# Optimization experiments

Measured on AMD Instinct MI355X. Metric: run time of the kernel, lower is better.

The kernel has to match this reference:

```python
import jax, jax.numpy as jnp
import numpy as np

EPS = 1e-5

def _bn(x, g, b):
    # training-mode BatchNorm3d over (N, T, H, W) per channel (axis=1), biased variance
    red = (0, 2, 3, 4)
    m = x.mean(red, keepdims=True)
    v = x.var(red, keepdims=True)
    s = (1, -1, 1, 1, 1)
    return (x - m) / jnp.sqrt(v + EPS) * g.reshape(s) + b.reshape(s)

def _conv3d(x, w, b):
    # Conv3d kernel (1,3,3), padding (0,1,1)
    y = jax.lax.conv_general_dilated(x, w, (1, 1, 1), ((0, 0), (1, 1), (1, 1)),
                                     dimension_numbers=('NCDHW', 'OIDHW', 'NCDHW'))
    return y + b[None, :, None, None, None]

def _forward(x1, x2, attn_weight, W_up, b_up, W_mlp, b_mlp, g_mlp, be_mlp,
             W_c1, b_c1, g_c1, be_c1, W_c2, b_c2, g_c2, be_c2):
    w2 = W_up[:, :, 0]  # [Cin, Cout, 2, 2]
    y = jnp.einsum('bcthw,cokl->bothkwl', x1, w2)
    b_, o, t, h, k, w_, l = y.shape
    x1u = y.reshape(b_, o, t, h * k, w_ * l) + b_up[None, :, None, None, None]

    bs, d_in, T, H, W = x2.shape
    nH = attn_weight.shape[0]
    hh, ww = attn_weight.shape[2], attn_weight.shape[3]
    # [nH, bs, h, w, T, T] -> [nH*bs, T*T, h, w], bilinear upsample to (H, W)
    A = attn_weight.transpose(0, 1, 4, 5, 2, 3).reshape(nH * bs, T * T, hh, ww)
    A = jax.image.resize(A, (nH * bs, T * T, H, W), method='linear')
    A = A.reshape(nH, bs, T, T, H, W)
    # per-(head,b,H,W) temporal attention matmul: avoids materializing x2.repeat(n_head,...)
    ctx = jnp.einsum('nbtsxy,bcsxy->btxycn', A, x2)  # [bs,T,H,W,d_in,nH]
    ctx = ctx.reshape(bs, T, H, W, d_in * nH)        # flatten order (c, n) matches torch permute+view
    hmlp = jnp.einsum('btxyk,ko->btxyo', ctx, W_mlp) + b_mlp
    hmlp = hmlp.transpose(0, 4, 1, 2, 3)  # [bs, enc, T, H, W]
    hmlp = jax.nn.relu(_bn(hmlp, g_mlp, be_mlp))

    x = jnp.concatenate([hmlp, x1u], axis=1)  # [bs, enc+dec, T, H, W]
    x = jax.nn.relu(_bn(_conv3d(x, W_c1, b_c1), g_c1, be_c1))
    x = jax.nn.relu(_bn(_conv3d(x, W_c2, b_c2), g_c2, be_c2))
    return x

def setup_inputs() -> dict:
    key = jax.random.key(0)
    ks = jax.random.split(key, 8)
    bs, T, H, W = 2, 8, 128, 128
    dec, enc, nH = 64, 32, 4
    hh = ww = 16  # attn_scale_factor = 8
    return {
        'x1': jax.random.normal(ks[0], (bs, dec, T, H // 2, W // 2), jnp.float32),
        'x2': jax.random.normal(ks[1], (bs, enc, T, H, W), jnp.float32),
        'attn_weight': jax.random.uniform(ks[2], (nH, bs, hh, ww, T, T), jnp.float32),
        'W_up': jax.random.normal(ks[3], (dec, dec, 1, 2, 2), jnp.float32) * 0.05,
        'b_up': jnp.zeros((dec,), jnp.float32),
        'W_mlp': jax.random.normal(ks[4], (nH * enc, enc), jnp.float32) * 0.05,
        'b_mlp': jnp.zeros((enc,), jnp.float32),
        'g_mlp': jnp.ones((enc,), jnp.float32),
        'be_mlp': jnp.zeros((enc,), jnp.float32),
        'W_c1': jax.random.normal(ks[5], (enc, dec + enc, 1, 3, 3), jnp.float32) * 0.05,
        'b_c1': jnp.zeros((enc,), jnp.float32),
        'g_c1': jnp.ones((enc,), jnp.float32),
        'be_c1': jnp.zeros((enc,), jnp.float32),
        'W_c2': jax.random.normal(ks[6], (enc, enc, 1, 3, 3), jnp.float32) * 0.05,
        'b_c2': jnp.zeros((enc,), jnp.float32),
        'g_c2': jnp.ones((enc,), jnp.float32),
        'be_c2': jnp.zeros((enc,), jnp.float32),
    }

def reference(x1, x2, attn_weight, W_up, b_up, W_mlp, b_mlp, g_mlp, be_mlp,
              W_c1, b_c1, g_c1, be_c1, W_c2, b_c2, g_c2, be_c2):
    return _forward(x1, x2, attn_weight, W_up, b_up, W_mlp, b_mlp, g_mlp, be_mlp,
                    W_c1, b_c1, g_c1, be_c1, W_c2, b_c2, g_c2, be_c2)
```

## Files before the change

### kernel.cpp

```cpp
#include <hip/hip_runtime.h>


#define EPSV 1e-5f

typedef __attribute__((ext_vector_type(8))) short short8;
typedef __attribute__((ext_vector_type(4))) short short4v;
typedef __attribute__((ext_vector_type(4))) float floatx4;

__device__ inline short f2bf(float f) {
  union { float f; unsigned u; } v; v.f = f;
  unsigned r = (v.u + 0x7fffu + ((v.u >> 16) & 1u)) >> 16;
  return (short)r;
}
__device__ inline float bf2f(short s) {
  union { unsigned u; float f; } v; v.u = ((unsigned)(unsigned short)s) << 16;
  return v.f;
}

#define UB_OFF   0
#define HMB_OFF  8388608
#define C1B_OFF  12582912
#define C2B_OFF  16777216
#define WB1_OFF  20971520
#define WB2_OFF  20985344
#define WUP_OFF  20989952
#define ST_OFF   20998144
#define SC_OFF   20998336

__global__ __launch_bounds__(256) void k_repackb(const float* __restrict__ Wc1, const float* __restrict__ Wc2,
        const float* __restrict__ Wup,
        short* __restrict__ wb1, short* __restrict__ wb2, short* __restrict__ wupb) {
  int i = blockIdx.x*256 + threadIdx.x;
  if (i < 27648) {
    int cc = i / 9216, r = i % 9216;
    int tap = r / 1024, r2 = r % 1024;
    int nt = r2 >> 9, lane = (r2 >> 3) & 63, j = r2 & 7;
    int o = nt*16 + (lane & 15);
    int cin = cc*32 + (lane >> 4)*8 + j;
    wb1[i] = f2bf(Wc1[(o*96 + cin)*9 + tap]);
  }
  if (i < 9216) {
    int tap = i / 1024, r2 = i % 1024;
    int nt = r2 >> 9, lane = (r2 >> 3) & 63, j = r2 & 7;
    int o = nt*16 + (lane & 15);
    int cin = (lane >> 4)*8 + j;
    wb2[i] = f2bf(Wc2[(o*32 + cin)*9 + tap]);
  }
  if (i < 16384) {
    int j = i & 7, lane = (i >> 3) & 63, r = i >> 9;
    int nt = r & 3, kb = (r >> 2) & 1, p = r >> 3;
    int c = kb*32 + (lane >> 4)*8 + j;
    int o = nt*16 + (lane & 15);
    wupb[i] = f2bf(Wup[(c*64 + o)*4 + p]);
  }
}

__global__ __launch_bounds__(256) void k_up_mfma(const float* __restrict__ x1,
        const short* __restrict__ wupb, const float* __restrict__ bup,
        short* __restrict__ Ub) {
  __shared__ __align__(16) char smem[34816];
  short8* stage = (short8*)smem;
  int t = blockIdx.y, b = blockIdx.z;
  int chunk = blockIdx.x >> 2, parity = blockIdx.x & 3;
  int tid = threadIdx.x, lane = tid & 63, w = tid >> 6;

  {
    const float* xp = x1 + ((long)(b*64)*8 + t)*4096 + chunk*256 + tid;
    #pragma unroll
    for (int o8 = 0; o8 < 8; ++o8) {
      short8 v;
      #pragma unroll
      for (int j = 0; j < 8; ++j) v[j] = f2bf(xp[(long)(o8*8+j)*32768]);
      int kb = o8 >> 2, cq = o8 & 3;
      stage[(kb*16 + (tid>>4))*64 + cq*16 + (tid&15)] = v;
    }
  }
  __syncthreads();

  floatx4 acc[4][4];
  #pragma unroll
  for (int nt=0; nt<4; ++nt) {
    float bb = bup[nt*16 + (lane&15)];
    #pragma unroll
    for (int mt=0; mt<4; ++mt) acc[mt][nt] = (floatx4){bb,bb,bb,bb};
  }
  const short8* wp = (const short8*)wupb;
  #pragma unroll
  for (int kb=0; kb<2; ++kb) {
    short8 bfr[4];
    #pragma unroll
    for (int nt=0; nt<4; ++nt) bfr[nt] = wp[((parity*2+kb)*4+nt)*64 + lane];
    #pragma unroll
    for (int mt=0; mt<4; ++mt) {
      short8 a = stage[(kb*16 + w*4 + mt)*64 + lane];
      #pragma unroll
      for (int nt=0; nt<4; ++nt)
        acc[mt][nt] = __builtin_amdgcn_mfma_f32_16x16x32_bf16(a, bfr[nt], acc[mt][nt], 0,0,0);
    }
  }

  __syncthreads();
  short* trb = (short*)smem;
  #pragma unroll
  for (int mt=0; mt<4; ++mt)
    #pragma unroll
    for (int nt=0; nt<4; ++nt)
      #pragma unroll
      for (int r=0; r<4; ++r)
        trb[(w*64 + mt*16 + (lane>>4)*4 + r)*68 + nt*16 + (lane&15)] = f2bf(acc[mt][nt][r]);
  __syncthreads();

  int ip = chunk*256 + tid;
  int X = 2*(ip>>6) + (parity>>1), Y = 2*(ip&63) + (parity&1);
  short* dst = Ub + (((long)(b*8+t)*16384 + X*128 + Y)*64);
  const short* src = trb + tid*68;
  #pragma unroll
  for (int k=0; k<16; ++k)
    *(short4v*)(dst + k*4) = *(const short4v*)(src + k*4);
}

__global__ __launch_bounds__(256) void k_ctxmlp(const float* __restrict__ x2,
        const float* __restrict__ attn, const float* __restrict__ Wmlp,
        const float* __restrict__ bmlp, short* __restrict__ HMb) {
  int t = blockIdx.y, b = blockIdx.z;
  int pos = blockIdx.x*256 + threadIdx.x;
  __shared__ float la[8192];
  float4* la4 = (float4*)la;
  const float4* g4 = (const float4*)attn;
  #pragma unroll
  for (int k=0;k<8;++k) {
    int i = k*256 + (int)threadIdx.x;
    int s4 = i & 1, iy = (i>>1)&15, ix = (i>>5)&15, n = i>>9;
    la4[i] = g4[((((n*2+b)*16+ix)*16+iy)*8+t)*2 + s4];
  }
  __syncthreads();
  int x = pos >> 7, y = pos & 127;
  float ux = (x+0.5f)*0.125f - 0.5f;
  float uy = (y+0.5f)*0.125f - 0.5f;
  int ix0 = (int)floorf(ux), iy0 = (int)floorf(uy);
  float fx = ux - (float)ix0, fy = uy - (float)iy0;
  int ixa = max(ix0,0), ixb = min(ix0+1,15);
  int iya = max(iy0,0), iyb = min(iy0+1,15);
  float w00=(1.f-fx)*(1.f-fy), w01=(1.f-fx)*fy, w10=fx*(1.f-fy), w11=fx*fy;
  float a[4][8];
  #pragma unroll
  for (int n=0;n<4;++n) {
    const float4* p00 = la4 + ((n*16+ixa)*16+iya)*2;
    const float4* p01 = la4 + ((n*16+ixa)*16+iyb)*2;
    const float4* p10 = la4 + ((n*16+ixb)*16+iya)*2;
    const float4* p11 = la4 + ((n*16+ixb)*16+iyb)*2;
    #pragma unroll
    for (int q=0;q<2;++q) {
      float4 c00=p00[q], c01=p01[q], c10=p10[q], c11=p11[q];
      a[n][q*4+0] = w00*c00.x + w01*c01.x + w10*c10.x + w11*c11.x;
      a[n][q*4+1] = w00*c00.y + w01*c01.y + w10*c10.y + w11*c11.y;
      a[n][q*4+2] = w00*c00.z + w01*c01.z + w10*c10.z + w11*c11.z;
      a[n][q*4+3] = w00*c00.w + w01*c01.w + w10*c10.w + w11*c11.w;
    }
  }
  float acc[32];
  #pragma unroll
  for (int o=0;o<32;++o) acc[o] = bmlp[o];
  const float* x2p = x2 + b*4194304 + pos;
  #pragma unroll 4
  for (int c=0;c<32;++c) {
    float xr[8];
    #pragma unroll
    for (int s=0;s<8;++s) xr[s] = x2p[(c*8+s)*16384];
    #pragma unroll
    for (int n=0;n<4;++n) {
      float ctx = 0.f;
      #pragma unroll
      for (int s=0;s<8;++s) ctx = fmaf(a[n][s], xr[s], ctx);
      const float* wrow = Wmlp + (c*4+n)*32;
      #pragma unroll
      for (int o=0;o<32;++o) acc[o] = fmaf(ctx, wrow[o], acc[o]);
    }
  }
  short8* hp = (short8*)(HMb + ((long)((b*8+t)*16384 + pos)) * 32);
  #pragma unroll
  for (int g=0; g<4; ++g) {
    short8 v;
    #pragma unroll
    for (int j=0;j<8;++j) v[j] = f2bf(acc[g*8+j]);
    hp[g] = v;
  }
}

__global__ __launch_bounds__(256) void k_stats_cl(const unsigned* __restrict__ src, float* __restrict__ st) {
  __shared__ float sb[64];
  if (threadIdx.x < 64) sb[threadIdx.x] = 0.f;
  __syncthreads();
  int cp = threadIdx.x & 15;
  int pg = threadIdx.x >> 4;
  long pbase = (long)blockIdx.x * 256;
  float s0=0.f,q0=0.f,s1=0.f,q1=0.f;
  #pragma unroll 4
  for (int it = 0; it < 16; ++it) {
    long pos = pbase + it*16 + pg;
    unsigned d = src[pos*16 + cp];
    float v0 = bf2f((short)(d & 0xffffu));
    float v1 = bf2f((short)(d >> 16));
    s0+=v0; q0+=v0*v0; s1+=v1; q1+=v1*v1;
  }
  s0 += __shfl_xor(s0,16); s0 += __shfl_xor(s0,32);
  q0 += __shfl_xor(q0,16); q0 += __shfl_xor(q0,32);
  s1 += __shfl_xor(s1,16); s1 += __shfl_xor(s1,32);
  q1 += __shfl_xor(q1,16); q1 += __shfl_xor(q1,32);
  if ((threadIdx.x & 63) < 16) {
    atomicAdd(&sb[2*cp],    s0); atomicAdd(&sb[2*cp+1],    s1);
    atomicAdd(&sb[32+2*cp], q0); atomicAdd(&sb[32+2*cp+1], q1);
  }
  __syncthreads();
  if (threadIdx.x < 64) atomicAdd(&st[threadIdx.x], sb[threadIdx.x]);
}

__global__ void k_finalize(const float* __restrict__ st, const float* __restrict__ g,
                           const float* __restrict__ be, float* __restrict__ sc, float* __restrict__ sh) {
  int c = threadIdx.x;
  if (c < 32) {
    float mean = st[c] * (1.f/262144.f);
    float var  = st[32+c] * (1.f/262144.f) - mean*mean;
    float s = g[c] / sqrtf(var + EPSV);
    sc[c] = s;
    sh[c] = be[c] - mean*s;
  }
}

template<int NCHUNK>
__global__ __launch_bounds__(256) void k_conv_mfma(
    const short* __restrict__ srcCL, const short* __restrict__ srcU,
    const short* __restrict__ wb, const float* __restrict__ bias,
    const float* __restrict__ sc, const float* __restrict__ sh,
    short* __restrict__ dstCL, float* __restrict__ st) {
  __shared__ __align__(16) char smem[25920];
  __shared__ float sbuf[64];
  short* stage = (short*)smem;

  int t = blockIdx.y, b = blockIdx.z;
  int x0 = (int)(blockIdx.x >> 3) * 16, y0 = (int)(blockIdx.x & 7) * 16;
  int tid = threadIdx.x, lane = tid & 63, w = tid >> 6;
  if (tid < 64) sbuf[tid] = 0.f;

  float bias0 = bias[lane & 15], bias1 = bias[16 + (lane & 15)];
  floatx4 acc[4][2];
  #pragma unroll
  for (int mt=0; mt<4; ++mt) {
    acc[mt][0] = (floatx4){bias0,bias0,bias0,bias0};
    acc[mt][1] = (floatx4){bias1,bias1,bias1,bias1};
  }
  long slab = (long)(b*8+t)*16384;

  for (int cc=0; cc<NCHUNK; ++cc) {
    __syncthreads();
    if (cc == 0) {
      #pragma unroll
      for (int g=0; g<4; ++g) {
        float s0=sc[g*8+0],s1=sc[g*8+1],s2=sc[g*8+2],s3=sc[g*8+3];
        float s4=sc[g*8+4],s5=sc[g*8+5],s6=sc[g*8+6],s7=sc[g*8+7];
        float h0=sh[g*8+0],h1=sh[g*8+1],h2=sh[g*8+2],h3=sh[g*8+3];
        float h4=sh[g*8+4],h5=sh[g*8+5],h6=sh[g*8+6],h7=sh[g*8+7];
        for (int p=tid; p<324; p+=256) {
          int r = p/18, c = p - r*18;
          int X = x0 - 1 + r, Y = y0 - 1 + c;
          short8 val = (short8)0;
          if ((unsigned)X < 128u && (unsigned)Y < 128u) {
            short8 raw = *(const short8*)(srcCL + ((slab + X*128 + Y) * 32 + g*8));
            val[0]=f2bf(fmaxf(fmaf(bf2f(raw[0]),s0,h0),0.f));
            val[1]=f2bf(fmaxf(fmaf(bf2f(raw[1]),s1,h1),0.f));
            val[2]=f2bf(fmaxf(fmaf(bf2f(raw[2]),s2,h2),0.f));
            val[3]=f2bf(fmaxf(fmaf(bf2f(raw[3]),s3,h3),0.f));
            val[4]=f2bf(fmaxf(fmaf(bf2f(raw[4]),s4,h4),0.f));
            val[5]=f2bf(fmaxf(fmaf(bf2f(raw[5]),s5,h5),0.f));
            val[6]=f2bf(fmaxf(fmaf(bf2f(raw[6]),s6,h6),0.f));
            val[7]=f2bf(fmaxf(fmaf(bf2f(raw[7]),s7,h7),0.f));
          }
          *(short8*)(stage + p*40 + g*8) = val;
        }
      }
    } else {
      int cbase = (cc-1)*32;
      #pragma unroll
      for (int g=0; g<4; ++g) {
        for (int p=tid; p<324; p+=256) {
          int r = p/18, c = p - r*18;
          int X = x0 - 1 + r, Y = y0 - 1 + c;
          short8 val = (short8)0;
          if ((unsigned)X < 128u && (unsigned)Y < 128u) {
            val = *(const short8*)(srcU + ((slab + X*128 + Y) * 64 + cbase + g*8));
          }
          *(short8*)(stage + p*40 + g*8) = val;
        }
      }
    }
    __syncthreads();
    const short8* wbp = (const short8*)wb + (long)cc*9*2*64;
    #pragma unroll
    for (int tap=0; tap<9; ++tap) {
      int dy = tap/3, dx = tap - dy*3;
      short8 b0 = wbp[(tap*2+0)*64 + lane];
      short8 b1 = wbp[(tap*2+1)*64 + lane];
      #pragma unroll
      for (int mt=0; mt<4; ++mt) {
        int p = (w*4 + mt + dy)*18 + (lane & 15) + dx;
        short8 a = *(const short8*)(stage + p*40 + (lane>>4)*8);
        acc[mt][0] = __builtin_amdgcn_mfma_f32_16x16x32_bf16(a, b0, acc[mt][0], 0,0,0);
        acc[mt][1] = __builtin_amdgcn_mfma_f32_16x16x32_bf16(a, b1, acc[mt][1], 0,0,0);
      }
    }
  }

  float s0=0.f,q0=0.f,s1=0.f,q1=0.f;
  #pragma unroll
  for (int mt=0; mt<4; ++mt)
    #pragma unroll
    for (int r=0; r<4; ++r) {
      float v0 = acc[mt][0][r]; s0 += v0; q0 += v0*v0;
      float v1 = acc[mt][1][r]; s1 += v1; q1 += v1*v1;
    }
  s0 += __shfl_xor(s0,16); s0 += __shfl_xor(s0,32);
  q0 += __shfl_xor(q0,16); q0 += __shfl_xor(q0,32);
  s1 += __shfl_xor(s1,16); s1 += __shfl_xor(s1,32);
  q1 += __shfl_xor(q1,16); q1 += __shfl_xor(q1,32);

  __syncthreads();
  if (lane < 16) {
    atomicAdd(&sbuf[lane],    s0); atomicAdd(&sbuf[16+lane], s1);
    atomicAdd(&sbuf[32+lane], q0); atomicAdd(&sbuf[48+lane], q1);
  }
  short* tr = (short*)smem;
  #pragma unroll
  for (int mt=0; mt<4; ++mt) {
    int prow = w*4 + mt;
    #pragma unroll
    for (int nt=0; nt<2; ++nt) {
      #pragma unroll
      for (int r=0; r<4; ++r) {
        int m = (lane>>4)*4 + r;
        tr[(prow*16 + m)*32 + nt*16 + (lane&15)] = f2bf(acc[mt][nt][r]);
      }
    }
  }
  __syncthreads();
  int px = tid >> 4, py = tid & 15;
  short8* d8 = (short8*)(dstCL + ((slab + (long)(x0+px)*128 + (y0+py))*32));
  const short8* s8 = (const short8*)(tr + tid*32);
  d8[0]=s8[0]; d8[1]=s8[1]; d8[2]=s8[2]; d8[3]=s8[3];
  if (tid < 64) atomicAdd(&st[tid], sbuf[tid]);
}

__global__ __launch_bounds__(256) void k_bnrelu2(const short* __restrict__ C2b,
        const float* __restrict__ sc, const float* __restrict__ sh,
        float* __restrict__ out) {
  __shared__ float tb[10592];
  int t = blockIdx.y, b = blockIdx.z;
  int posbase = blockIdx.x * 256;
  int tid = threadIdx.x;
  long slab = (long)(b*8+t)*16384;
  {
    const short8* sp = (const short8*)(C2b + (slab + posbase + tid)*32);
    int pi = tid + (tid>>5)*8;
    #pragma unroll
    for (int g=0; g<4; ++g) {
      short8 v = sp[g];
      #pragma unroll
      for (int j=0; j<8; ++j) {
        int ch = g*8+j;
        tb[ch*321 + pi] = fmaxf(fmaf(bf2f(v[j]), sc[ch], sh[ch]), 0.f);
      }
    }
  }
  __syncthreads();
  int ch = tid >> 3, pg = tid & 7;
  float* op = out + ((long)(b*32+ch)*8 + t)*16384 + posbase + pg*32;
  const float* tp = tb + ch*321 + pg*40;
  #pragma unroll
  for (int k=0; k<8; ++k) {
    float4 v;
    v.x = tp[k*4+0]; v.y = tp[k*4+1]; v.z = tp[k*4+2]; v.w = tp[k*4+3];
    *(float4*)(op + k*4) = v;
  }
}

extern "C" void kernel_launch(void* const* d_in, const int* in_sizes, int n_in,
                              void* d_out, int out_size, void* d_ws, size_t ws_size,
                              hipStream_t stream) {
  (void)in_sizes; (void)n_in; (void)out_size; (void)ws_size;
  const float* x1   = (const float*)d_in[0];
  const float* x2   = (const float*)d_in[1];
  const float* attn = (const float*)d_in[2];
  const float* Wup  = (const float*)d_in[3];
  const float* bup  = (const float*)d_in[4];
  const float* Wmlp = (const float*)d_in[5];
  const float* bmlp = (const float*)d_in[6];
  const float* gmlp = (const float*)d_in[7];
  const float* bemlp= (const float*)d_in[8];
  const float* Wc1  = (const float*)d_in[9];
  const float* bc1  = (const float*)d_in[10];
  const float* gc1  = (const float*)d_in[11];
  const float* bec1 = (const float*)d_in[12];
  const float* Wc2  = (const float*)d_in[13];
  const float* bc2  = (const float*)d_in[14];
  const float* gc2  = (const float*)d_in[15];
  const float* bec2 = (const float*)d_in[16];
  float* ws  = (float*)d_ws;
  float* out = (float*)d_out;

  short* Ub   = (short*)(ws + UB_OFF);
  short* HMb  = (short*)(ws + HMB_OFF);
  short* C1b  = (short*)(ws + C1B_OFF);
  short* C2b  = (short*)(ws + C2B_OFF);
  short* wb1  = (short*)(ws + WB1_OFF);
  short* wb2  = (short*)(ws + WB2_OFF);
  short* wupb = (short*)(ws + WUP_OFF);
  float* st1  = ws + ST_OFF;
  float* st2  = st1 + 64;
  float* st3  = st2 + 64;
  float* sc1  = ws + SC_OFF;  float* sh1 = sc1+32;
  float* sc2  = sh1+32;       float* sh2 = sc2+32;
  float* sc3  = sh2+32;       float* sh3 = sc3+32;

  hipMemsetAsync(st1, 0, 192*sizeof(float), stream);
  k_repackb<<<108, 256, 0, stream>>>(Wc1, Wc2, Wup, wb1, wb2, wupb);
  k_up_mfma<<<dim3(64,8,2), 256, 0, stream>>>(x1, wupb, bup, Ub);
  k_ctxmlp<<<dim3(64,8,2), 256, 0, stream>>>(x2, attn, Wmlp, bmlp, HMb);
  k_stats_cl<<<1024, 256, 0, stream>>>((const unsigned*)HMb, st1);
  k_finalize<<<1, 32, 0, stream>>>(st1, gmlp, bemlp, sc1, sh1);
  k_conv_mfma<3><<<dim3(64,8,2), 256, 0, stream>>>(HMb, Ub, wb1, bc1, sc1, sh1, C1b, st2);
  k_finalize<<<1, 32, 0, stream>>>(st2, gc1, bec1, sc2, sh2);
  k_conv_mfma<1><<<dim3(64,8,2), 256, 0, stream>>>(C1b, nullptr, wb2, bc2, sc2, sh2, C2b, st3);
  k_finalize<<<1, 32, 0, stream>>>(st3, gc2, bec2, sc3, sh3);
  k_bnrelu2<<<dim3(64,8,2), 256, 0, stream>>>(C2b, sc3, sh3, out);
}
```

Before: 322.9 us.

## Fuse BN stats into ctxmlp, split BN apply, load conv operands directly

The BN1 statistics pass moves into the ctx/MLP kernel through a shared-memory transpose, which removes the separate stats kernel that re-read HMb. BN+ReLU is now applied by standalone elementwise kernels that write normalized bf16 copies (HMn, C1n). The conv kernels read their A operands straight from global memory per tap instead of staging a halo tile in LDS, and each block covers a 2x128 row strip instead of a 16x16 tile. This trades extra launches, extra buffer round-trips and about nine redundant global loads per element for fewer syncs and no LDS staging.

Measured after the change: 371.0 us. 14.9% more time.

```diff
diff --git a/kernel.cpp b/kernel.cpp
--- a/kernel.cpp
+++ b/kernel.cpp
@@ -19,13 +19,15 @@
 
 #define UB_OFF   0
 #define HMB_OFF  8388608
-#define C1B_OFF  12582912
-#define C2B_OFF  16777216
-#define WB1_OFF  20971520
-#define WB2_OFF  20985344
-#define WUP_OFF  20989952
-#define ST_OFF   20998144
-#define SC_OFF   20998336
+#define HMN_OFF  12582912
+#define C1B_OFF  16777216
+#define C1N_OFF  20971520
+#define C2B_OFF  25165824
+#define WB1_OFF  29360128
+#define WB2_OFF  29373952
+#define WUP_OFF  29378560
+#define ST_OFF   29386752
+#define SC_OFF   29386944
 
 __global__ __launch_bounds__(256) void k_repackb(const float* __restrict__ Wc1, const float* __restrict__ Wc2,
         const float* __restrict__ Wup,
@@ -121,15 +123,18 @@
 
 __global__ __launch_bounds__(256) void k_ctxmlp(const float* __restrict__ x2,
         const float* __restrict__ attn, const float* __restrict__ Wmlp,
-        const float* __restrict__ bmlp, short* __restrict__ HMb) {
+        const float* __restrict__ bmlp, short* __restrict__ HMb, float* __restrict__ st) {
+  __shared__ float la[8448];
+  __shared__ float sb[64];
   int t = blockIdx.y, b = blockIdx.z;
-  int pos = blockIdx.x*256 + threadIdx.x;
-  __shared__ float la[8192];
+  int tid = threadIdx.x, lane = tid & 63;
+  int pos = blockIdx.x*256 + tid;
+  if (tid < 64) sb[tid] = 0.f;
   float4* la4 = (float4*)la;
   const float4* g4 = (const float4*)attn;
   #pragma unroll
   for (int k=0;k<8;++k) {
-    int i = k*256 + (int)threadIdx.x;
+    int i = k*256 + tid;
     int s4 = i & 1, iy = (i>>1)&15, ix = (i>>5)&15, n = i>>9;
     la4[i] = g4[((((n*2+b)*16+ix)*16+iy)*8+t)*2 + s4];
   }
@@ -185,34 +190,18 @@
     for (int j=0;j<8;++j) v[j] = f2bf(acc[g*8+j]);
     hp[g] = v;
   }
-}
-
-__global__ __launch_bounds__(256) void k_stats_cl(const unsigned* __restrict__ src, float* __restrict__ st) {
-  __shared__ float sb[64];
-  if (threadIdx.x < 64) sb[threadIdx.x] = 0.f;
-  __syncthreads();
-  int cp = threadIdx.x & 15;
-  int pg = threadIdx.x >> 4;
-  long pbase = (long)blockIdx.x * 256;
-  float s0=0.f,q0=0.f,s1=0.f,q1=0.f;
-  #pragma unroll 4
-  for (int it = 0; it < 16; ++it) {
-    long pos = pbase + it*16 + pg;
-    unsigned d = src[pos*16 + cp];
-    float v0 = bf2f((short)(d & 0xffffu));
-    float v1 = bf2f((short)(d >> 16));
-    s0+=v0; q0+=v0*v0; s1+=v1; q1+=v1*v1;
-  }
-  s0 += __shfl_xor(s0,16); s0 += __shfl_xor(s0,32);
-  q0 += __shfl_xor(q0,16); q0 += __shfl_xor(q0,32);
-  s1 += __shfl_xor(s1,16); s1 += __shfl_xor(s1,32);
-  q1 += __shfl_xor(q1,16); q1 += __shfl_xor(q1,32);
-  if ((threadIdx.x & 63) < 16) {
-    atomicAdd(&sb[2*cp],    s0); atomicAdd(&sb[2*cp+1],    s1);
-    atomicAdd(&sb[32+2*cp], q0); atomicAdd(&sb[32+2*cp+1], q1);
-  }
-  __syncthreads();
-  if (threadIdx.x < 64) atomicAdd(&st[threadIdx.x], sb[threadIdx.x]);
+  __syncthreads();
+  #pragma unroll
+  for (int c=0;c<32;++c) la[tid*33 + c] = acc[c];
+  __syncthreads();
+  int ch = tid & 31, grp = tid >> 5;
+  float s = 0.f, q = 0.f;
+  #pragma unroll 8
+  for (int p=0;p<32;++p) { float v = la[(grp*32+p)*33 + ch]; s += v; q += v*v; }
+  s += __shfl_xor(s, 32); q += __shfl_xor(q, 32);
+  if (lane < 32) { atomicAdd(&sb[ch], s); atomicAdd(&sb[32+ch], q); }
+  __syncthreads();
+  if (tid < 64) atomicAdd(&st[tid], sb[tid]);
 }
 
 __global__ void k_finalize(const float* __restrict__ st, const float* __restrict__ g,
@@ -227,83 +216,64 @@
   }
 }
 
+__global__ __launch_bounds__(256) void k_bnapply(const short* __restrict__ src,
+        const float* __restrict__ sc, const float* __restrict__ sh, short* __restrict__ dst) {
+  long i = (long)blockIdx.x*256 + threadIdx.x;
+  const short8* sp = (const short8*)(src + i*32);
+  short8* dp = (short8*)(dst + i*32);
+  #pragma unroll
+  for (int g=0; g<4; ++g) {
+    short8 v = sp[g], o;
+    #pragma unroll
+    for (int j=0;j<8;++j)
+      o[j] = f2bf(fmaxf(fmaf(bf2f(v[j]), sc[g*8+j], sh[g*8+j]), 0.f));
+    dp[g] = o;
+  }
+}
+
 template<int NCHUNK>
-__global__ __launch_bounds__(256) void k_conv_mfma(
-    const short* __restrict__ srcCL, const short* __restrict__ srcU,
+__global__ __launch_bounds__(256) void k_convd(
+    const short* __restrict__ src0, const short* __restrict__ src1,
     const short* __restrict__ wb, const float* __restrict__ bias,
-    const float* __restrict__ sc, const float* __restrict__ sh,
     short* __restrict__ dstCL, float* __restrict__ st) {
-  __shared__ __align__(16) char smem[25920];
+  __shared__ __align__(16) short tr[256*32];
   __shared__ float sbuf[64];
-  short* stage = (short*)smem;
-
   int t = blockIdx.y, b = blockIdx.z;
-  int x0 = (int)(blockIdx.x >> 3) * 16, y0 = (int)(blockIdx.x & 7) * 16;
   int tid = threadIdx.x, lane = tid & 63, w = tid >> 6;
   if (tid < 64) sbuf[tid] = 0.f;
-
-  float bias0 = bias[lane & 15], bias1 = bias[16 + (lane & 15)];
+  long slab = (long)(b*8+t)*16384;
+  int pbase = blockIdx.x * 256;
+  int x0 = pbase >> 7;
+  int m = lane & 15, kg = lane >> 4;
+
+  float bias0 = bias[m], bias1 = bias[16 + m];
   floatx4 acc[4][2];
   #pragma unroll
   for (int mt=0; mt<4; ++mt) {
     acc[mt][0] = (floatx4){bias0,bias0,bias0,bias0};
     acc[mt][1] = (floatx4){bias1,bias1,bias1,bias1};
   }
-  long slab = (long)(b*8+t)*16384;
-
+
+  #pragma unroll
   for (int cc=0; cc<NCHUNK; ++cc) {
-    __syncthreads();
-    if (cc == 0) {
-      #pragma unroll
-      for (int g=0; g<4; ++g) {
-        float s0=sc[g*8+0],s1=sc[g*8+1],s2=sc[g*8+2],s3=sc[g*8+3];
-        float s4=sc[g*8+4],s5=sc[g*8+5],s6=sc[g*8+6],s7=sc[g*8+7];
-        float h0=sh[g*8+0],h1=sh[g*8+1],h2=sh[g*8+2],h3=sh[g*8+3];
-        float h4=sh[g*8+4],h5=sh[g*8+5],h6=sh[g*8+6],h7=sh[g*8+7];
-        for (int p=tid; p<324; p+=256) {
-          int r = p/18, c = p - r*18;
-          int X = x0 - 1 + r, Y = y0 - 1 + c;
-          short8 val = (short8)0;
-          if ((unsigned)X < 128u && (unsigned)Y < 128u) {
-            short8 raw = *(const short8*)(srcCL + ((slab + X*128 + Y) * 32 + g*8));
-            val[0]=f2bf(fmaxf(fmaf(bf2f(raw[0]),s0,h0),0.f));
-            val[1]=f2bf(fmaxf(fmaf(bf2f(raw[1]),s1,h1),0.f));
-            val[2]=f2bf(fmaxf(fmaf(bf2f(raw[2]),s2,h2),0.f));
-            val[3]=f2bf(fmaxf(fmaf(bf2f(raw[3]),s3,h3),0.f));
-            val[4]=f2bf(fmaxf(fmaf(bf2f(raw[4]),s4,h4),0.f));
-            val[5]=f2bf(fmaxf(fmaf(bf2f(raw[5]),s5,h5),0.f));
-            val[6]=f2bf(fmaxf(fmaf(bf2f(raw[6]),s6,h6),0.f));
-            val[7]=f2bf(fmaxf(fmaf(bf2f(raw[7]),s7,h7),0.f));
-          }
-          *(short8*)(stage + p*40 + g*8) = val;
-        }
-      }
-    } else {
-      int cbase = (cc-1)*32;
-      #pragma unroll
-      for (int g=0; g<4; ++g) {
-        for (int p=tid; p<324; p+=256) {
-          int r = p/18, c = p - r*18;
-          int X = x0 - 1 + r, Y = y0 - 1 + c;
-          short8 val = (short8)0;
-          if ((unsigned)X < 128u && (unsigned)Y < 128u) {
-            val = *(const short8*)(srcU + ((slab + X*128 + Y) * 64 + cbase + g*8));
-          }
-          *(short8*)(stage + p*40 + g*8) = val;
-        }
-      }
-    }
-    __syncthreads();
+    const short* sbase = (cc==0) ? src0 : src1;
+    const int cstr = (cc==0) ? 32 : 64;
+    const int coff = (cc==0) ? 0 : (cc-1)*32;
     const short8* wbp = (const short8*)wb + (long)cc*9*2*64;
     #pragma unroll
     for (int tap=0; tap<9; ++tap) {
-      int dy = tap/3, dx = tap - dy*3;
+      int dy = tap/3, dx = tap - 3*dy;
       short8 b0 = wbp[(tap*2+0)*64 + lane];
       short8 b1 = wbp[(tap*2+1)*64 + lane];
       #pragma unroll
       for (int mt=0; mt<4; ++mt) {
-        int p = (w*4 + mt + dy)*18 + (lane & 15) + dx;
-        short8 a = *(const short8*)(stage + p*40 + (lane>>4)*8);
+        int tile = w*4 + mt;
+        int row = x0 + (tile >> 3);
+        int X = row + dy - 1;
+        int Y = (tile & 7)*16 + m + dx - 1;
+        short8 a = (short8)0;
+        if (((unsigned)X < 128u) & ((unsigned)Y < 128u))
+          a = *(const short8*)(sbase + (slab + X*128 + Y)*cstr + coff + kg*8);
         acc[mt][0] = __builtin_amdgcn_mfma_f32_16x16x32_bf16(a, b0, acc[mt][0], 0,0,0);
         acc[mt][1] = __builtin_amdgcn_mfma_f32_16x16x32_bf16(a, b1, acc[mt][1], 0,0,0);
       }
@@ -322,28 +292,24 @@
   q0 += __shfl_xor(q0,16); q0 += __shfl_xor(q0,32);
   s1 += __shfl_xor(s1,16); s1 += __shfl_xor(s1,32);
   q1 += __shfl_xor(q1,16); q1 += __shfl_xor(q1,32);
-
-  __syncthreads();
   if (lane < 16) {
     atomicAdd(&sbuf[lane],    s0); atomicAdd(&sbuf[16+lane], s1);
     atomicAdd(&sbuf[32+lane], q0); atomicAdd(&sbuf[48+lane], q1);
   }
-  short* tr = (short*)smem;
+
   #pragma unroll
   for (int mt=0; mt<4; ++mt) {
-    int prow = w*4 + mt;
-    #pragma unroll
-    for (int nt=0; nt<2; ++nt) {
+    int tile = w*4 + mt;
+    #pragma unroll
+    for (int nt=0; nt<2; ++nt)
       #pragma unroll
       for (int r=0; r<4; ++r) {
-        int m = (lane>>4)*4 + r;
-        tr[(prow*16 + m)*32 + nt*16 + (lane&15)] = f2bf(acc[mt][nt][r]);
+        int pin = kg*4 + r;
+        tr[(tile*16 + pin)*32 + nt*16 + m] = f2bf(acc[mt][nt][r]);
       }
-    }
-  }
-  __syncthreads();
-  int px = tid >> 4, py = tid & 15;
-  short8* d8 = (short8*)(dstCL + ((slab + (long)(x0+px)*128 + (y0+py))*32));
+  }
+  __syncthreads();
+  short8* d8 = (short8*)(dstCL + (slab + pbase + tid)*32);
   const short8* s8 = (const short8*)(tr + tid*32);
   d8[0]=s8[0]; d8[1]=s8[1]; d8[2]=s8[2]; d8[3]=s8[3];
   if (tid < 64) atomicAdd(&st[tid], sbuf[tid]);
@@ -408,7 +374,9 @@
 
   short* Ub   = (short*)(ws + UB_OFF);
   short* HMb  = (short*)(ws + HMB_OFF);
+  short* HMn  = (short*)(ws + HMN_OFF);
   short* C1b  = (short*)(ws + C1B_OFF);
+  short* C1n  = (short*)(ws + C1N_OFF);
   short* C2b  = (short*)(ws + C2B_OFF);
   short* wb1  = (short*)(ws + WB1_OFF);
   short* wb2  = (short*)(ws + WB2_OFF);
@@ -423,12 +391,13 @@
   hipMemsetAsync(st1, 0, 192*sizeof(float), stream);
   k_repackb<<<108, 256, 0, stream>>>(Wc1, Wc2, Wup, wb1, wb2, wupb);
   k_up_mfma<<<dim3(64,8,2), 256, 0, stream>>>(x1, wupb, bup, Ub);
-  k_ctxmlp<<<dim3(64,8,2), 256, 0, stream>>>(x2, attn, Wmlp, bmlp, HMb);
-  k_stats_cl<<<1024, 256, 0, stream>>>((const unsigned*)HMb, st1);
+  k_ctxmlp<<<dim3(64,8,2), 256, 0, stream>>>(x2, attn, Wmlp, bmlp, HMb, st1);
   k_finalize<<<1, 32, 0, stream>>>(st1, gmlp, bemlp, sc1, sh1);
-  k_conv_mfma<3><<<dim3(64,8,2), 256, 0, stream>>>(HMb, Ub, wb1, bc1, sc1, sh1, C1b, st2);
+  k_bnapply<<<1024, 256, 0, stream>>>(HMb, sc1, sh1, HMn);
+  k_convd<3><<<dim3(64,8,2), 256, 0, stream>>>(HMn, Ub, wb1, bc1, C1b, st2);
   k_finalize<<<1, 32, 0, stream>>>(st2, gc1, bec1, sc2, sh2);
-  k_conv_mfma<1><<<dim3(64,8,2), 256, 0, stream>>>(C1b, nullptr, wb2, bc2, sc2, sh2, C2b, st3);
+  k_bnapply<<<1024, 256, 0, stream>>>(C1b, sc2, sh2, C1n);
+  k_convd<1><<<dim3(64,8,2), 256, 0, stream>>>(C1n, nullptr, wb2, bc2, C2b, st3);
   k_finalize<<<1, 32, 0, stream>>>(st3, gc2, bec2, sc3, sh3);
   k_bnrelu2<<<dim3(64,8,2), 256, 0, stream>>>(C2b, sc3, sh3, out);
 }
```
